# Kernel optimization log

Hardware: AMD Instinct MI355X
Metric: run time of the kernel (lower is better)

## Reference

```python
import jax, jax.numpy as jnp
import numpy as np

V = 32          # num_variables
T = 48          # num_time_bins
D = 512         # d_model
H = 8           # num_heads
HD = D // H     # head_dim = 64
OD = 16         # observation_dim
B = 4


def setup_inputs() -> dict:
    key = jax.random.key(0)
    ks = jax.random.split(key, 20)
    s = 0.02
    inp = {
        'h': jax.random.normal(ks[0], (B, T, V, D), jnp.float32),
        'observation_state': jax.random.normal(ks[1], (B, T, V, 2), jnp.float32),
        'Wq': jax.random.normal(ks[2], (D, D), jnp.float32) * s,
        'bq': jnp.zeros((D,), jnp.float32),
        'Wk': jax.random.normal(ks[3], (D, D), jnp.float32) * s,
        'bk': jnp.zeros((D,), jnp.float32),
        'Wv': jax.random.normal(ks[4], (D, D), jnp.float32) * s,
        'bv': jnp.zeros((D,), jnp.float32),
        'Wo': jax.random.normal(ks[5], (D, D), jnp.float32) * s,
        'bo': jnp.zeros((D,), jnp.float32),
        'Woq': jax.random.normal(ks[6], (2, H * OD), jnp.float32) * 0.5,
        'boq': jnp.zeros((H * OD,), jnp.float32),
        'Wok': jax.random.normal(ks[7], (2, H * OD), jnp.float32) * 0.5,
        'bok': jnp.zeros((H * OD,), jnp.float32),
        'variable_bias': jax.random.normal(ks[8], (H, V, V), jnp.float32) * 0.01,
        'relative_time_bias': jax.random.normal(ks[9], (H, 2 * T - 1), jnp.float32) * 0.01,
    }
    return inp


def reference(h, observation_state, Wq, bq, Wk, bk, Wv, bv, Wo, bo,
              Woq, boq, Wok, bok, variable_bias, relative_time_bias):
    N = T * V
    scale = 1.0 / np.sqrt(HD)
    obs_scale = 1.0 / np.sqrt(OD)

    # static index buffers (constants)
    flat_var_ids = jnp.tile(jnp.arange(V), T)                       # [N]
    flat_time_ids = jnp.repeat(jnp.arange(T), V)                    # [N]
    rel_index = flat_time_ids[:, None] - flat_time_ids[None, :] + (T - 1)  # [N,N]

    fh = h.reshape(B, N, D)
    fo = observation_state.reshape(B, N, 2)

    def heads(x, nh, hd):
        return x.reshape(B, N, nh, hd).transpose(0, 2, 1, 3)  # [B,H,N,hd]

    q = heads(fh @ Wq + bq, H, HD)
    k = heads(fh @ Wk + bk, H, HD)
    v = heads(fh @ Wv + bv, H, HD)
    oq = heads(fo @ Woq + boq, H, OD)
    ok = heads(fo @ Wok + bok, H, OD)

    content = jnp.einsum('bhnd,bhmd->bhnm', q, k) * scale
    obs = jnp.einsum('bhnd,bhmd->bhnm', oq, ok) * obs_scale
    var_scores = variable_bias[:, flat_var_ids[:, None], flat_var_ids[None, :]]  # [H,N,N]
    time_scores = relative_time_bias[:, rel_index]                                # [H,N,N]

    scores = content + obs + var_scores[None] + time_scores[None]
    attn = jax.nn.softmax(scores, axis=-1)  # dropout off (inference)
    out = jnp.einsum('bhnm,bhmd->bhnd', attn, v)
    out = out.transpose(0, 2, 1, 3).reshape(B, N, D)
    out = out @ Wo + bo
    return out.reshape(B, T, V, D)
```

## Files before the change

kernel.cpp:

```cpp
#include <hip/hip_runtime.h>
#include <math.h>

typedef __bf16 bf16x8 __attribute__((ext_vector_type(8)));
typedef float f32x4 __attribute__((ext_vector_type(4)));

#define NB 4
#define NT 48
#define NV 32
#define ND 512
#define NH 8
#define NN 1536
#define NBN 6144
#define L2E 1.44269504f

#define GLOAD_LDS(g, l) \
    __builtin_amdgcn_global_load_lds( \
        (const __attribute__((address_space(1))) void*)(g), \
        (__attribute__((address_space(3))) void*)(l), 16, 0, 0)

__global__ __launch_bounds__(256) void prep(
    const float* __restrict__ h, const float* __restrict__ obs,
    const float* __restrict__ Wq, const float* __restrict__ Wk,
    const float* __restrict__ Wv, const float* __restrict__ Wo,
    const float* __restrict__ bq, const float* __restrict__ bk,
    const float* __restrict__ bv,
    const float* __restrict__ Wok, const float* __restrict__ bok,
    __bf16* __restrict__ h_bf, __bf16* __restrict__ WcatT,
    __bf16* __restrict__ WoT, float* __restrict__ biascat,
    __bf16* __restrict__ kx)
{
    __shared__ float ts[64][68];
    const int tid = threadIdx.x;
    const int bx = blockIdx.x;
    if (bx < 1536) {
        int t = bx * 256 + tid;
        const float4* src = (const float4*)h + (size_t)t * 2;
        float4 a = src[0], b = src[1];
        __bf16 r[8] = {(__bf16)a.x, (__bf16)a.y, (__bf16)a.z, (__bf16)a.w,
                       (__bf16)b.x, (__bf16)b.y, (__bf16)b.z, (__bf16)b.w};
        *(uint4*)(h_bf + (size_t)t * 8) = *(uint4*)r;
    } else if (bx < 1792) {
        int bw = bx - 1536;
        const int p = bw >> 6, tile = bw & 63;
        const int k0 = (tile >> 3) * 64, c0 = (tile & 7) * 64;
        const float* W = (p == 0) ? Wq : (p == 1) ? Wk : (p == 2) ? Wv : Wo;
        const float scale = (p == 0) ? 0.125f * L2E : 1.0f;
        #pragma unroll
        for (int i = 0; i < 4; i++) {
            int r = (tid >> 4) + i * 16;
            float4 v = *(const float4*)(W + (size_t)(k0 + r) * 512 + c0 + (tid & 15) * 4);
            *(float4*)&ts[r][(tid & 15) * 4] = v;
        }
        __syncthreads();
        __bf16 tmp[16];
        #pragma unroll
        for (int j = 0; j < 16; j++)
            tmp[j] = (__bf16)(ts[(tid & 3) * 16 + j][tid >> 2] * scale);
        int crow = c0 + (tid >> 2);
        __bf16* dst = (p < 3)
            ? WcatT + ((size_t)(p * 512 + crow)) * 512 + k0 + (tid & 3) * 16
            : WoT   + ((size_t)crow) * 512 + k0 + (tid & 3) * 16;
        *(uint4*)dst = *(uint4*)tmp;
        *(uint4*)(dst + 8) = *(uint4*)(tmp + 8);
        if (p < 3 && k0 == 0 && tid < 64) {
            const float* bb = (p == 0) ? bq : (p == 1) ? bk : bv;
            biascat[p * 512 + c0 + tid] = bb[c0 + tid] * scale;
        }
    } else {
        int t = (bx - 1792) * 256 + tid;
        int row = t >> 1, half = t & 1;
        __bf16* dst = kx + (size_t)row * 96 + 64 + half * 16;
        if (half == 0) {
            int bh = row / NN, n = row - bh * NN;
            int b = bh >> 3, hh = bh & 7;
            size_t bn = (size_t)b * NN + n;
            float o0 = obs[bn * 2], o1 = obs[bn * 2 + 1];
            int f = hh * 16;
            __bf16 tmp[16];
            #pragma unroll
            for (int j = 0; j < 16; j++)
                tmp[j] = (__bf16)(o0 * Wok[f + j] + o1 * Wok[128 + f + j] + bok[f + j]);
            *(uint4*)dst       = *(uint4*)tmp;
            *(uint4*)(dst + 8) = *(uint4*)(tmp + 8);
        } else {
            uint4 z = {0, 0, 0, 0};
            *(uint4*)dst       = z;
            *(uint4*)(dst + 8) = z;
        }
    }
}

template<int TM, bool BF16OUT>
__global__ __launch_bounds__(256) void gemm_mfma(
    const __bf16* __restrict__ A, const __bf16* __restrict__ Bt,
    const float* __restrict__ bias, float* __restrict__ Cf,
    __bf16* __restrict__ qarr, __bf16* __restrict__ kx,
    __bf16* __restrict__ vt)
{
    constexpr int MT = TM / 32;
    __shared__ __align__(16) char smem[34816];
    __bf16 (*As)[32] = (__bf16(*)[32])smem;
    __bf16 (*Bs)[32] = (__bf16(*)[32])(smem + TM * 64);
    const int tid = threadIdx.x;
    const int w = tid >> 6, lane = tid & 63;
    const int quad = lane >> 4, l16 = lane & 15;
    const int wm = w >> 1, wn = w & 1;
    const int n0 = blockIdx.x * 128, m0 = blockIdx.y * TM;

    const int sm = tid >> 2;
    const int sk = ((tid & 3) ^ ((sm >> 1) & 3)) * 8;
    const __bf16* aptr = A  + (size_t)(m0 + sm) * 512 + sk;
    const __bf16* bptr = Bt + (size_t)(n0 + sm) * 512 + sk;
    __bf16* lA = (__bf16*)As + tid * 8;
    __bf16* lB = (__bf16*)Bs + tid * 8;

    f32x4 zero4 = {0.f, 0.f, 0.f, 0.f};
    f32x4 acc[MT][4];
    #pragma unroll
    for (int i = 0; i < MT; i++)
        #pragma unroll
        for (int j = 0; j < 4; j++) acc[i][j] = zero4;

    for (int kt = 0; kt < 512; kt += 32) {
        __syncthreads();
        GLOAD_LDS(aptr + kt, lA);
        if (TM == 128) GLOAD_LDS(aptr + 64 * 512 + kt, lA + 2048);
        GLOAD_LDS(bptr + kt, lB);
        GLOAD_LDS(bptr + 64 * 512 + kt, lB + 2048);
        __syncthreads();
        bf16x8 af[MT], bfr[4];
        #pragma unroll
        for (int mt = 0; mt < MT; mt++) {
            int rr = wm * (TM / 2) + mt * 16 + l16;
            af[mt] = *(const bf16x8*)&As[rr][(quad ^ ((rr >> 1) & 3)) * 8];
        }
        #pragma unroll
        for (int nt = 0; nt < 4; nt++) {
            int rr = wn * 64 + nt * 16 + l16;
            bfr[nt] = *(const bf16x8*)&Bs[rr][(quad ^ ((rr >> 1) & 3)) * 8];
        }
        #pragma unroll
        for (int mt = 0; mt < MT; mt++)
            #pragma unroll
            for (int nt = 0; nt < 4; nt++)
                acc[mt][nt] = __builtin_amdgcn_mfma_f32_16x16x32_bf16(
                    af[mt], bfr[nt], acc[mt][nt], 0, 0, 0);
    }

    __syncthreads();
    if (BF16OUT) {
        if (n0 >= 1024) {
            __bf16* CsT = (__bf16*)smem;
            #pragma unroll
            for (int nt = 0; nt < 4; nt++) {
                int cl = wn * 64 + nt * 16 + l16;
                float bia = bias[n0 + cl];
                #pragma unroll
                for (int mt = 0; mt < MT; mt++) {
                    int rl0 = wm * (TM / 2) + mt * 16 + quad * 4;
                    __bf16 pk[4];
                    #pragma unroll
                    for (int r = 0; r < 4; r++)
                        pk[r] = (__bf16)(acc[mt][nt][r] + bia);
                    *(uint2*)&CsT[cl * 136 + rl0] = *(uint2*)pk;
                }
            }
            __syncthreads();
            int cl = tid >> 1, half = tid & 1;
            int f0 = (n0 + cl) & 511;
            int hh = f0 >> 6, d = f0 & 63;
            int bidx = m0 / NN, nm = m0 - bidx * NN;
            __bf16* dst = vt + ((size_t)(bidx * 8 + hh) * 64 + d) * 1536
                             + nm + half * 64;
            #pragma unroll
            for (int j = 0; j < 8; j++) {
                uint4 v = *(uint4*)&CsT[cl * 136 + half * 64 + j * 8];
                *(uint4*)(dst + j * 8) = v;
            }
        } else {
            __bf16* Cs = (__bf16*)smem;
            #pragma unroll
            for (int mt = 0; mt < MT; mt++)
                #pragma unroll
                for (int nt = 0; nt < 4; nt++) {
                    int cl = wn * 64 + nt * 16 + l16;
                    float bia = bias[n0 + cl];
                    #pragma unroll
                    for (int r = 0; r < 4; r++) {
                        int rl = wm * (TM / 2) + mt * 16 + quad * 4 + r;
                        Cs[rl * 132 + cl] = (__bf16)(acc[mt][nt][r] + bia);
                    }
                }
            __syncthreads();
            int rl = tid >> 1, hb = tid & 1;
            int grow = m0 + rl;
            int col0 = n0 + hb * 64;
            int p = col0 >> 9, f0 = col0 & 511, hh = f0 >> 6;
            int bidx = grow / NN, n = grow - bidx * NN;
            __bf16* dst = (p == 0) ? qarr + (size_t)grow * 512 + f0
                                   : kx + ((size_t)(bidx * 8 + hh) * NN + n) * 96;
            #pragma unroll
            for (int j = 0; j < 8; j++) {
                uint2 lo = *(uint2*)&Cs[rl * 132 + hb * 64 + j * 8];
                uint2 hi = *(uint2*)&Cs[rl * 132 + hb * 64 + j * 8 + 4];
                uint4 v = {lo.x, lo.y, hi.x, hi.y};
                *(uint4*)(dst + j * 8) = v;
            }
        }
    } else {
        float* Csf = (float*)smem;
        #pragma unroll
        for (int mt = 0; mt < MT; mt++)
            #pragma unroll
            for (int nt = 0; nt < 4; nt++) {
                int cl = wn * 64 + nt * 16 + l16;
                float bia = bias[n0 + cl];
                #pragma unroll
                for (int r = 0; r < 4; r++) {
                    int rl = wm * (TM / 2) + mt * 16 + quad * 4 + r;
                    Csf[rl * 132 + cl] = acc[mt][nt][r] + bia;
                }
            }
        __syncthreads();
        int rl = tid >> 2, q4 = tid & 3;
        float* dst = Cf + (size_t)(m0 + rl) * 512 + n0 + q4 * 32;
        #pragma unroll
        for (int j = 0; j < 8; j++) {
            uint4 v = *(uint4*)&Csf[rl * 132 + q4 * 32 + j * 4];
            *(uint4*)(dst + j * 4) = v;
        }
    }
}

__global__ __launch_bounds__(256) void attn_mfma(
    const __bf16* __restrict__ qarr, const __bf16* __restrict__ kx,
    const __bf16* __restrict__ vt, const float* __restrict__ obs,
    const float* __restrict__ Woq, const float* __restrict__ boq,
    const float* __restrict__ varb, const float* __restrict__ rtb,
    __bf16* __restrict__ aout)
{
    __shared__ __align__(16) __bf16 Ks[64][128];
    __shared__ __align__(16) __bf16 Vs[64][64];
    __shared__ __align__(16) __bf16 Ps[64][64];
    __shared__ float rts[96];

    const int tid = threadIdx.x;
    const int w = tid >> 6, lane = tid & 63;
    const int quad = lane >> 4, l16 = lane & 15;
    const int bh = blockIdx.x, qt = blockIdx.y;
    const int b = bh >> 3, h = bh & 7;
    const int n0 = qt * 64;

    if (tid < 95) rts[tid] = rtb[h * 95 + tid] * L2E;

    const int nl = w * 16 + l16;
    const size_t qrow = (size_t)(b * NN + n0 + nl);
    bf16x8 bq_[3];
    bq_[0] = *(const bf16x8*)(qarr + qrow * 512 + h * 64 + quad * 8);
    bq_[1] = *(const bf16x8*)(qarr + qrow * 512 + h * 64 + 32 + quad * 8);
    {
        uint4 a2u = {0u, 0u, 0u, 0u};
        if (quad < 2) {
            float o0 = obs[qrow * 2], o1 = obs[qrow * 2 + 1];
            int f = h * 16 + quad * 8;
            const float sc = 0.25f * L2E;
            __bf16 tmp[8];
            #pragma unroll
            for (int j = 0; j < 8; j++)
                tmp[j] = (__bf16)(sc * (o0 * Woq[f + j] + o1 * Woq[128 + f + j]
                                        + boq[f + j]));
            a2u = *(uint4*)tmp;
        }
        bq_[2] = *(bf16x8*)&a2u;
    }

    const int rm = (w & 1) * 16 + l16;
    float4 vbA = *(const float4*)(varb + h * 1024 + rm * 32 + quad * 4);
    float4 vbB = *(const float4*)(varb + h * 1024 + rm * 32 + 16 + quad * 4);
    float vA[4] = {vbA.x * L2E, vbA.y * L2E, vbA.z * L2E, vbA.w * L2E};
    float vB[4] = {vbB.x * L2E, vbB.y * L2E, vbB.z * L2E, vbB.w * L2E};
    const int tn = 2 * qt + (w >> 1);

    const int ck = (tid & 15) ^ ((tid >> 4) & 7);
    const __bf16* kbase = kx + (size_t)bh * NN * 96 + ck * 8;
    const int cv = (tid & 7) ^ ((tid >> 3) & 7);
    const __bf16* vbase = vt + (size_t)bh * 64 * 1536 + cv * 8;

    int wo2[4], ro2[2];
    #pragma unroll
    for (int ct = 0; ct < 4; ct++)
        wo2[ct] = (((ct * 2 + (quad >> 1)) ^ (nl & 7)) * 16) + (quad & 1) * 8;
    #pragma unroll
    for (int ks = 0; ks < 2; ks++)
        ro2[ks] = ((ks * 4 + quad) ^ (nl & 7)) * 16;
    char* psrow = (char*)Ps + nl * 128;

    f32x4 zero4 = {0.f, 0.f, 0.f, 0.f};
    f32x4 o[4];
    float lp = 0.f;
    #pragma unroll
    for (int i = 0; i < 4; i++) o[i] = zero4;

    char* ldsK = (char*)Ks;
    char* ldsV = (char*)Vs;

    for (int mt = 0; mt < 24; mt++) {
        const int m0 = mt * 64;
        __syncthreads();
        #pragma unroll
        for (int i = 0; i < 4; i++) {
            int row = i * 16 + (tid >> 4);
            GLOAD_LDS(kbase + (size_t)(m0 + row) * 96, ldsK + i * 4096 + tid * 16);
        }
        #pragma unroll
        for (int i = 0; i < 2; i++) {
            int row = i * 32 + (tid >> 3);
            GLOAD_LDS(vbase + (size_t)row * 1536 + m0, ldsV + i * 4096 + tid * 16);
        }
        __syncthreads();

        f32x4 sc[4];
        #pragma unroll
        for (int ct = 0; ct < 4; ct++) {
            f32x4 d = zero4;
            int row = ct * 16 + l16;
            #pragma unroll
            for (int ks = 0; ks < 3; ks++) {
                bf16x8 kf = *(const bf16x8*)((const char*)Ks + row * 256
                                + (((ks * 4 + quad) ^ (row & 7)) * 16));
                d = __builtin_amdgcn_mfma_f32_16x16x32_bf16(kf, bq_[ks], d, 0, 0, 0);
            }
            sc[ct] = d;
        }
        float tb0 = rts[tn - 2 * mt + 47];
        float tb1 = rts[tn - 2 * mt + 46];
        #pragma unroll
        for (int ct = 0; ct < 4; ct++) {
            float tb = (ct & 2) ? tb1 : tb0;
            const float* vv = (ct & 1) ? vB : vA;
            __bf16 pk[4];
            #pragma unroll
            for (int r = 0; r < 4; r++) {
                float p = exp2f(sc[ct][r] + tb + vv[r]);
                lp += p;
                pk[r] = (__bf16)p;
            }
            *(uint2*)(psrow + wo2[ct]) = *(uint2*)pk;
        }
        #pragma unroll
        for (int ks = 0; ks < 2; ks++) {
            bf16x8 pf = *(const bf16x8*)(psrow + ro2[ks]);
            #pragma unroll
            for (int dt = 0; dt < 4; dt++) {
                int rw = dt * 16 + l16;
                bf16x8 vf = *(const bf16x8*)((const char*)Vs + rw * 128
                                + (((ks * 4 + quad) ^ (rw & 7)) * 16));
                o[dt] = __builtin_amdgcn_mfma_f32_16x16x32_bf16(vf, pf, o[dt], 0, 0, 0);
            }
        }
    }

    lp += __shfl_xor(lp, 16);
    lp += __shfl_xor(lp, 32);
    float inv = 1.0f / lp;
    size_t abase = ((size_t)b * NN + n0 + nl) * 512 + h * 64 + quad * 4;
    #pragma unroll
    for (int dt = 0; dt < 4; dt++) {
        __bf16 ov[4];
        #pragma unroll
        for (int r = 0; r < 4; r++) ov[r] = (__bf16)(o[dt][r] * inv);
        *(uint2*)(aout + abase + dt * 16) = *(uint2*)ov;
    }
}

extern "C" void kernel_launch(void* const* d_in, const int* in_sizes, int n_in,
                              void* d_out, int out_size, void* d_ws, size_t ws_size,
                              hipStream_t stream)
{
    const float* h_   = (const float*)d_in[0];
    const float* obs  = (const float*)d_in[1];
    const float* Wq   = (const float*)d_in[2];
    const float* bq   = (const float*)d_in[3];
    const float* Wk   = (const float*)d_in[4];
    const float* bk   = (const float*)d_in[5];
    const float* Wv   = (const float*)d_in[6];
    const float* bv   = (const float*)d_in[7];
    const float* Wo   = (const float*)d_in[8];
    const float* bo   = (const float*)d_in[9];
    const float* Woq  = (const float*)d_in[10];
    const float* boq  = (const float*)d_in[11];
    const float* Wok  = (const float*)d_in[12];
    const float* bok  = (const float*)d_in[13];
    const float* varb = (const float*)d_in[14];
    const float* rtb  = (const float*)d_in[15];
    float* out = (float*)d_out;

    char* ws = (char*)d_ws;
    __bf16* h_bf    = (__bf16*)ws;                 ws += (size_t)NBN * 512 * 2;
    __bf16* qarr    = (__bf16*)ws;                 ws += (size_t)NBN * 512 * 2;
    __bf16* vt      = (__bf16*)ws;                 ws += (size_t)NBN * 512 * 2;
    __bf16* kx      = (__bf16*)ws;                 ws += ((size_t)32 * NN * 96 + 64) * 2;
    __bf16* attnout = (__bf16*)ws;                 ws += (size_t)NBN * 512 * 2;
    __bf16* WcatT   = (__bf16*)ws;                 ws += (size_t)1536 * 512 * 2;
    __bf16* WoT     = (__bf16*)ws;                 ws += (size_t)512 * 512 * 2;
    float*  biascat = (float*)ws;                  ws += 1536 * 4;

    prep<<<dim3(2176), dim3(256), 0, stream>>>(
        h_, obs, Wq, Wk, Wv, Wo, bq, bk, bv, Wok, bok,
        h_bf, WcatT, WoT, biascat, kx);
    gemm_mfma<128, true><<<dim3(12, 48), dim3(256), 0, stream>>>(
        h_bf, WcatT, biascat, nullptr, qarr, kx, vt);
    attn_mfma<<<dim3(32, 24), dim3(256), 0, stream>>>(qarr, kx, vt, obs, Woq, boq,
                                                      varb, rtb, attnout);
    gemm_mfma<64, false><<<dim3(4, 96), dim3(256), 0, stream>>>(
        attnout, WoT, bo, out, nullptr, nullptr, nullptr);
}
```

Measured before the change: 180.6 us.

## Double-buffer LDS tiles in GEMM and attention kernels to overlap loads

Both the projection GEMM and the attention kernel now use two LDS buffers. The next K/V (or A/B) tile is issued with global_load_lds while the current tile is being computed, which replaces the two barriers per iteration with one wait plus barrier. The attention kernel also raises wave priority around its MFMA sections and keeps the softmax row-sum in four accumulators instead of one serial chain. The cost is more LDS in the attention kernel, which may lower occupancy, and the vmcnt waits are hand-placed.

```diff
diff --git a/kernel.cpp b/kernel.cpp
--- a/kernel.cpp
+++ b/kernel.cpp
@@ -99,8 +99,10 @@
 {
     constexpr int MT = TM / 32;
     __shared__ __align__(16) char smem[34816];
-    __bf16 (*As)[32] = (__bf16(*)[32])smem;
-    __bf16 (*Bs)[32] = (__bf16(*)[32])(smem + TM * 64);
+    char* const As0 = smem;
+    char* const As1 = smem + TM * 64;
+    char* const Bs0 = smem + TM * 128;
+    char* const Bs1 = smem + TM * 128 + 8192;
     const int tid = threadIdx.x;
     const int w = tid >> 6, lane = tid & 63;
     const int quad = lane >> 4, l16 = lane & 15;
@@ -111,8 +113,6 @@
     const int sk = ((tid & 3) ^ ((sm >> 1) & 3)) * 8;
     const __bf16* aptr = A  + (size_t)(m0 + sm) * 512 + sk;
     const __bf16* bptr = Bt + (size_t)(n0 + sm) * 512 + sk;
-    __bf16* lA = (__bf16*)As + tid * 8;
-    __bf16* lB = (__bf16*)Bs + tid * 8;
 
     f32x4 zero4 = {0.f, 0.f, 0.f, 0.f};
     f32x4 acc[MT][4];
@@ -121,23 +121,23 @@
         #pragma unroll
         for (int j = 0; j < 4; j++) acc[i][j] = zero4;
 
-    for (int kt = 0; kt < 512; kt += 32) {
-        __syncthreads();
-        GLOAD_LDS(aptr + kt, lA);
-        if (TM == 128) GLOAD_LDS(aptr + 64 * 512 + kt, lA + 2048);
-        GLOAD_LDS(bptr + kt, lB);
-        GLOAD_LDS(bptr + 64 * 512 + kt, lB + 2048);
-        __syncthreads();
+    auto STAGE = [&](char* dA, char* dB, int kt) {
+        GLOAD_LDS(aptr + kt, dA + tid * 16);
+        if (TM == 128) GLOAD_LDS(aptr + 64 * 512 + kt, dA + 4096 + tid * 16);
+        GLOAD_LDS(bptr + kt, dB + tid * 16);
+        GLOAD_LDS(bptr + 64 * 512 + kt, dB + 4096 + tid * 16);
+    };
+    auto COMPUTE = [&](const char* Asb, const char* Bsb) {
         bf16x8 af[MT], bfr[4];
         #pragma unroll
         for (int mt = 0; mt < MT; mt++) {
             int rr = wm * (TM / 2) + mt * 16 + l16;
-            af[mt] = *(const bf16x8*)&As[rr][(quad ^ ((rr >> 1) & 3)) * 8];
+            af[mt] = *(const bf16x8*)(Asb + rr * 64 + (quad ^ ((rr >> 1) & 3)) * 16);
         }
         #pragma unroll
         for (int nt = 0; nt < 4; nt++) {
             int rr = wn * 64 + nt * 16 + l16;
-            bfr[nt] = *(const bf16x8*)&Bs[rr][(quad ^ ((rr >> 1) & 3)) * 8];
+            bfr[nt] = *(const bf16x8*)(Bsb + rr * 64 + (quad ^ ((rr >> 1) & 3)) * 16);
         }
         #pragma unroll
         for (int mt = 0; mt < MT; mt++)
@@ -145,6 +145,20 @@
             for (int nt = 0; nt < 4; nt++)
                 acc[mt][nt] = __builtin_amdgcn_mfma_f32_16x16x32_bf16(
                     af[mt], bfr[nt], acc[mt][nt], 0, 0, 0);
+    };
+
+    STAGE(As0, Bs0, 0);
+    asm volatile("s_waitcnt vmcnt(0)" ::: "memory");
+    __builtin_amdgcn_s_barrier();
+    for (int kt = 0; kt < 512; kt += 64) {
+        STAGE(As1, Bs1, kt + 32);
+        COMPUTE(As0, Bs0);
+        asm volatile("s_waitcnt vmcnt(0)" ::: "memory");
+        __builtin_amdgcn_s_barrier();
+        if (kt + 64 < 512) STAGE(As0, Bs0, kt + 64);
+        COMPUTE(As1, Bs1);
+        asm volatile("s_waitcnt vmcnt(0)" ::: "memory");
+        __builtin_amdgcn_s_barrier();
     }
 
     __syncthreads();
@@ -239,8 +253,10 @@
     const float* __restrict__ varb, const float* __restrict__ rtb,
     __bf16* __restrict__ aout)
 {
-    __shared__ __align__(16) __bf16 Ks[64][128];
-    __shared__ __align__(16) __bf16 Vs[64][64];
+    __shared__ __align__(16) __bf16 Ks0[64][128];
+    __shared__ __align__(16) __bf16 Ks1[64][128];
+    __shared__ __align__(16) __bf16 Vs0[64][64];
+    __shared__ __align__(16) __bf16 Vs1[64][64];
     __shared__ __align__(16) __bf16 Ps[64][64];
     __shared__ float rts[96];
 
@@ -252,6 +268,26 @@
     const int n0 = qt * 64;
 
     if (tid < 95) rts[tid] = rtb[h * 95 + tid] * L2E;
+
+    const int ck = (tid & 15) ^ ((tid >> 4) & 7);
+    const __bf16* kbase = kx + (size_t)bh * NN * 96 + ck * 8;
+    const int cv = (tid & 7) ^ ((tid >> 3) & 7);
+    const __bf16* vbase = vt + (size_t)bh * 64 * 1536 + cv * 8;
+
+    auto STAGE = [&](char* dk, char* dv, int m0s) {
+        #pragma unroll
+        for (int i = 0; i < 4; i++) {
+            int row = i * 16 + (tid >> 4);
+            GLOAD_LDS(kbase + (size_t)(m0s + row) * 96, dk + i * 4096 + tid * 16);
+        }
+        #pragma unroll
+        for (int i = 0; i < 2; i++) {
+            int row = i * 32 + (tid >> 3);
+            GLOAD_LDS(vbase + (size_t)row * 1536 + m0s, dv + i * 4096 + tid * 16);
+        }
+    };
+
+    STAGE((char*)Ks0, (char*)Vs0, 0);
 
     const int nl = w * 16 + l16;
     const size_t qrow = (size_t)(b * NN + n0 + nl);
@@ -281,11 +317,6 @@
     float vB[4] = {vbB.x * L2E, vbB.y * L2E, vbB.z * L2E, vbB.w * L2E};
     const int tn = 2 * qt + (w >> 1);
 
-    const int ck = (tid & 15) ^ ((tid >> 4) & 7);
-    const __bf16* kbase = kx + (size_t)bh * NN * 96 + ck * 8;
-    const int cv = (tid & 7) ^ ((tid >> 3) & 7);
-    const __bf16* vbase = vt + (size_t)bh * 64 * 1536 + cv * 8;
-
     int wo2[4], ro2[2];
     #pragma unroll
     for (int ct = 0; ct < 4; ct++)
@@ -297,43 +328,28 @@
 
     f32x4 zero4 = {0.f, 0.f, 0.f, 0.f};
     f32x4 o[4];
-    float lp = 0.f;
+    f32x4 lpv = zero4;
     #pragma unroll
     for (int i = 0; i < 4; i++) o[i] = zero4;
 
-    char* ldsK = (char*)Ks;
-    char* ldsV = (char*)Vs;
-
-    for (int mt = 0; mt < 24; mt++) {
-        const int m0 = mt * 64;
-        __syncthreads();
-        #pragma unroll
-        for (int i = 0; i < 4; i++) {
-            int row = i * 16 + (tid >> 4);
-            GLOAD_LDS(kbase + (size_t)(m0 + row) * 96, ldsK + i * 4096 + tid * 16);
-        }
-        #pragma unroll
-        for (int i = 0; i < 2; i++) {
-            int row = i * 32 + (tid >> 3);
-            GLOAD_LDS(vbase + (size_t)row * 1536 + m0, ldsV + i * 4096 + tid * 16);
-        }
-        __syncthreads();
-
+    auto COMPUTE = [&](const char* Kb, const char* Vb, int mti) {
         f32x4 sc[4];
+        __builtin_amdgcn_s_setprio(1);
         #pragma unroll
         for (int ct = 0; ct < 4; ct++) {
             f32x4 d = zero4;
             int row = ct * 16 + l16;
             #pragma unroll
             for (int ks = 0; ks < 3; ks++) {
-                bf16x8 kf = *(const bf16x8*)((const char*)Ks + row * 256
+                bf16x8 kf = *(const bf16x8*)(Kb + row * 256
                                 + (((ks * 4 + quad) ^ (row & 7)) * 16));
                 d = __builtin_amdgcn_mfma_f32_16x16x32_bf16(kf, bq_[ks], d, 0, 0, 0);
             }
             sc[ct] = d;
         }
-        float tb0 = rts[tn - 2 * mt + 47];
-        float tb1 = rts[tn - 2 * mt + 46];
+        __builtin_amdgcn_s_setprio(0);
+        float tb0 = rts[tn - 2 * mti + 47];
+        float tb1 = rts[tn - 2 * mti + 46];
         #pragma unroll
         for (int ct = 0; ct < 4; ct++) {
             float tb = (ct & 2) ? tb1 : tb0;
@@ -342,24 +358,41 @@
             #pragma unroll
             for (int r = 0; r < 4; r++) {
                 float p = exp2f(sc[ct][r] + tb + vv[r]);
-                lp += p;
+                lpv[r] += p;
                 pk[r] = (__bf16)p;
             }
             *(uint2*)(psrow + wo2[ct]) = *(uint2*)pk;
         }
+        __builtin_amdgcn_s_setprio(1);
         #pragma unroll
         for (int ks = 0; ks < 2; ks++) {
             bf16x8 pf = *(const bf16x8*)(psrow + ro2[ks]);
             #pragma unroll
             for (int dt = 0; dt < 4; dt++) {
                 int rw = dt * 16 + l16;
-                bf16x8 vf = *(const bf16x8*)((const char*)Vs + rw * 128
+                bf16x8 vf = *(const bf16x8*)(Vb + rw * 128
                                 + (((ks * 4 + quad) ^ (rw & 7)) * 16));
                 o[dt] = __builtin_amdgcn_mfma_f32_16x16x32_bf16(vf, pf, o[dt], 0, 0, 0);
             }
         }
-    }
-
+        __builtin_amdgcn_s_setprio(0);
+    };
+
+    asm volatile("s_waitcnt vmcnt(0) lgkmcnt(0)" ::: "memory");
+    __builtin_amdgcn_s_barrier();
+
+    for (int mt = 0; mt < 24; mt += 2) {
+        STAGE((char*)Ks1, (char*)Vs1, (mt + 1) * 64);
+        COMPUTE((const char*)Ks0, (const char*)Vs0, mt);
+        asm volatile("s_waitcnt vmcnt(0)" ::: "memory");
+        __builtin_amdgcn_s_barrier();
+        if (mt + 2 < 24) STAGE((char*)Ks0, (char*)Vs0, (mt + 2) * 64);
+        COMPUTE((const char*)Ks1, (const char*)Vs1, mt + 1);
+        asm volatile("s_waitcnt vmcnt(0)" ::: "memory");
+        __builtin_amdgcn_s_barrier();
+    }
+
+    float lp = (lpv[0] + lpv[1]) + (lpv[2] + lpv[3]);
     lp += __shfl_xor(lp, 16);
     lp += __shfl_xor(lp, 32);
     float inv = 1.0f / lp;
```

Result: slower. 190.2 us (+5.3%).
